# Performance work log

Measured on AMD Instinct MI355X. Metric: run time of the kernel, lower is better.

## Reference

```python
import jax, jax.numpy as jnp
import numpy as np
from jax import ops

N, E, F_IN, H, M, KC, B, C_OUT = 100000, 1600000, 128, 128, 150000, 60000, 64, 10
BN_EPS = 1e-5

def setup_inputs() -> dict:
    key = jax.random.key(0)
    ks = jax.random.split(key, 16)
    s = 0.05
    x = jax.random.normal(ks[0], (N, F_IN), jnp.float32)
    edge_index = jax.random.randint(ks[1], (2, E), 0, N)
    weights = jax.random.uniform(ks[2], (E,), jnp.float32)
    # sorted batch vector covering all B graphs
    batch = (jnp.arange(N) * B) // N
    # cover assignments: every cluster gets at least one node (arange prefix)
    cover_nodes = jax.random.randint(ks[3], (M,), 0, N)
    cover_clusters = jnp.concatenate([jnp.arange(KC), jax.random.randint(ks[4], (M - KC,), 0, KC)])
    cluster_batch = (jnp.arange(KC) * B) // KC
    out_dim = 4 * H  # 2 * num_layers * hidden, readout=True
    return {
        'x': x, 'edge_index': edge_index, 'weights': weights, 'batch': batch,
        'cover_nodes': cover_nodes, 'cover_clusters': cover_clusters, 'cluster_batch': cluster_batch,
        'W_in': jax.random.normal(ks[5], (F_IN, H), jnp.float32) * s,
        'b_in': jnp.zeros((H,), jnp.float32),
        'W_blk': jax.random.normal(ks[6], (2 * H, H), jnp.float32) * s,
        'b_blk': jnp.zeros((H,), jnp.float32),
        'bn_gamma': jnp.ones((out_dim,), jnp.float32),
        'bn_beta': jnp.zeros((out_dim,), jnp.float32),
        'bn_mean': jnp.zeros((out_dim,), jnp.float32),
        'bn_var': jnp.ones((out_dim,), jnp.float32),
        'W1': jax.random.normal(ks[7], (out_dim, H), jnp.float32) * s,
        'b1': jnp.zeros((H,), jnp.float32),
        'W2': jax.random.normal(ks[8], (H, C_OUT), jnp.float32) * s,
        'b2': jnp.zeros((C_OUT,), jnp.float32),
    }

def _gcn(x, src, dst, w, n, W, b):
    # PyG GCNConv: out = D^-1/2 (A + I) D^-1/2 (x W) + b, weighted degrees incl. self loop of 1
    deg = ops.segment_sum(w, dst, num_segments=n) + 1.0
    dinv = jax.lax.rsqrt(deg)
    xw = x @ W
    msg = (w * dinv[src] * dinv[dst])[:, None] * xw[src]          # [E,H]
    agg = ops.segment_sum(msg, dst, num_segments=n) + (dinv * dinv)[:, None] * xw
    return agg + b

def reference(x, edge_index, weights, batch, cover_nodes, cover_clusters, cluster_batch,
              W_in, b_in, W_blk, b_blk, bn_gamma, bn_beta, bn_mean, bn_var, W1, b1, W2, b2):
    src, dst = edge_index[0], edge_index[1]

    # conv_in + relu
    h = jax.nn.relu(_gcn(x, src, dst, weights, N, W_in, b_in))     # [N,H]

    counts = ops.segment_sum(jnp.ones((N,), jnp.float32), batch, num_segments=B)
    xs = [ops.segment_sum(h, batch, num_segments=B),               # global_add_pool
          ops.segment_max(h, batch, num_segments=B)]               # global_max_pool

    # --- pool_graphs: cover_pool_node (add & max) ---
    x_add = ops.segment_sum(h[cover_nodes], cover_clusters, num_segments=KC)
    x_max = ops.segment_max(h[cover_nodes], cover_clusters, num_segments=KC)
    xp = jnp.concatenate([x_add, x_max], axis=1)                   # [KC, 2H]

    # --- pooled GCN, matrix-free A' = C^T A C (cover_pool_edge, pool='add') ---
    def aprime(z):  # z: [KC, d]
        zn = ops.segment_sum(z[cover_clusters], cover_nodes, num_segments=N)   # C z
        ye = ops.segment_sum(weights[:, None] * zn[src], dst, num_segments=N)  # A (C z)
        return ops.segment_sum(ye[cover_nodes], cover_clusters, num_segments=KC)  # C^T ...

    degp = aprime(jnp.ones((KC, 1), jnp.float32))[:, 0] + 1.0      # weighted degree of A'+I
    dinv = jax.lax.rsqrt(degp)
    xw = xp @ W_blk                                                # [KC,H]
    xws = dinv[:, None] * xw
    hp = jax.nn.relu(dinv[:, None] * (aprime(xws) + xws) + b_blk)  # [KC,H]

    ccounts = ops.segment_sum(jnp.ones((KC,), jnp.float32), cluster_batch, num_segments=B)
    xs.append(ops.segment_sum(hp, cluster_batch, num_segments=B) / ccounts[:, None])  # mean pool
    xs.append(ops.segment_max(hp, cluster_batch, num_segments=B))

    z = jnp.concatenate(xs, axis=1)                                # [B, 4H]
    z = (z - bn_mean) * jax.lax.rsqrt(bn_var + BN_EPS) * bn_gamma + bn_beta  # BN (eval)
    z = jax.nn.relu(z @ W1 + b1)                                   # dropout=identity (eval)
    z = z @ W2 + b2
    return jax.nn.softmax(z, axis=-1)
```

## Files before the change

### kernel.cpp

```cpp
#include <hip/hip_runtime.h>


#define H 128
#define TILE_AGG 2048
#define GRID_AGG 784

typedef __attribute__((ext_vector_type(4))) float f32x4;
typedef __attribute__((ext_vector_type(8))) short bf16x8;

__device__ __forceinline__ void atomAddF(float* p, float v) {
    unsafeAtomicAdd(p, v);
}
__device__ __forceinline__ void atomMaxPos(float* p, float v) {
    atomicMax(reinterpret_cast<int*>(p), __float_as_int(v));
}

__device__ __forceinline__ unsigned int bfr(float f) {
    unsigned int u = __float_as_uint(f);
    return (u + 0x7fffu + ((u >> 16) & 1u)) >> 16;
}
__device__ __forceinline__ unsigned int pk2(float lo, float hi) {
    return bfr(lo) | (bfr(hi) << 16);
}
__device__ __forceinline__ float unlo(unsigned int v) { return __uint_as_float(v << 16); }
__device__ __forceinline__ float unhi(unsigned int v) { return __uint_as_float(v & 0xffff0000u); }

__global__ void count_pairs(const int* __restrict__ a, const int* __restrict__ b,
                            int* __restrict__ ca, int* __restrict__ cb, int M) {
    int i = blockIdx.x * blockDim.x + threadIdx.x;
    if (i < M) {
        atomicAdd(&ca[__builtin_nontemporal_load(a + i)], 1);
        atomicAdd(&cb[__builtin_nontemporal_load(b + i)], 1);
    }
}

__global__ __launch_bounds__(256) void scan_partial(const int* __restrict__ c,
                                                    int* __restrict__ part, int m) {
    __shared__ int red[4];
    int base = blockIdx.x * 1024, t = threadIdx.x;
    int s = 0;
    for (int j = t; j < 1024; j += 256) { int i = base + j; if (i < m) s += c[i]; }
    for (int o = 32; o; o >>= 1) s += __shfl_down(s, o, 64);
    if ((t & 63) == 0) red[t >> 6] = s;
    __syncthreads();
    if (t == 0) part[blockIdx.x] = red[0] + red[1] + red[2] + red[3];
}
__global__ void scan_spine(int* part, int G) {
    if (threadIdx.x == 0) {
        int acc = 0;
        for (int i = 0; i < G; ++i) { int v = part[i]; part[i] = acc; acc += v; }
    }
}
__global__ __launch_bounds__(256) void scan_apply(int* __restrict__ c,
                                                  const int* __restrict__ part, int m) {
    __shared__ int wsum[4];
    int base = blockIdx.x * 1024, t = threadIdx.x;
    int i0 = base + t * 4;
    int v0 = 0, v1 = 0, v2 = 0, v3 = 0;
    if (i0     < m) v0 = c[i0];
    if (i0 + 1 < m) v1 = c[i0 + 1];
    if (i0 + 2 < m) v2 = c[i0 + 2];
    if (i0 + 3 < m) v3 = c[i0 + 3];
    int ts = v0 + v1 + v2 + v3;
    int lane = t & 63, w = t >> 6;
    int sc = ts;
    for (int o = 1; o < 64; o <<= 1) { int u = __shfl_up(sc, o, 64); if (lane >= o) sc += u; }
    if (lane == 63) wsum[w] = sc;
    __syncthreads();
    int off = part[blockIdx.x];
    for (int k = 0; k < w; ++k) off += wsum[k];
    int ex = off + sc - ts;
    if (i0     < m) c[i0]     = ex;
    if (i0 + 1 < m) c[i0 + 1] = ex + v0;
    if (i0 + 2 < m) c[i0 + 2] = ex + v0 + v1;
    if (i0 + 3 < m) c[i0 + 3] = ex + v0 + v1 + v2;
}

__global__ void fill_pairs(const int* __restrict__ key, const int* __restrict__ val,
                           int* __restrict__ offs, int* __restrict__ slots, int M) {
    int i = blockIdx.x * blockDim.x + threadIdx.x;
    int p0 = i * 2, p1 = p0 + 1;
    if (p0 >= M) return;
    int k0 = __builtin_nontemporal_load(key + p0);
    int v0 = __builtin_nontemporal_load(val + p0);
    bool has1 = p1 < M;
    int k1 = k0, v1 = 0;
    if (has1) {
        k1 = __builtin_nontemporal_load(key + p1);
        v1 = __builtin_nontemporal_load(val + p1);
    }
    int q0 = atomicAdd(&offs[k0], 1);
    int q1 = has1 ? atomicAdd(&offs[k1], 1) : 0;
    slots[q0] = v0;
    if (has1) slots[q1] = v1;
}

__global__ void qcnt_kernel(const int* __restrict__ qoffs, int* __restrict__ qcnt, int N) {
    int n = blockIdx.x * blockDim.x + threadIdx.x;
    if (n < N) qcnt[n] = qoffs[n] - (n ? qoffs[n - 1] : 0);
}

__global__ __launch_bounds__(256) void hist_coarse(const int* __restrict__ dst,
                                                   int* __restrict__ histc, int E, int Ppad) {
    __shared__ int hb[512];
    for (int i = threadIdx.x; i < 512; i += 256) hb[i] = 0;
    __syncthreads();
    int x = blockIdx.x & 7;
    for (int tile = blockIdx.x; (long)tile * TILE_AGG < E; tile += GRID_AGG) {
        int base = tile * TILE_AGG;
        int lim = min(TILE_AGG, E - base);
        for (int i = threadIdx.x; i < lim; i += 256)
            atomicAdd(&hb[__builtin_nontemporal_load(dst + base + i) >> 8], 1);
    }
    __syncthreads();
    for (int i = threadIdx.x; i < 512; i += 256)
        if (hb[i]) atomicAdd(&histc[x * Ppad + i], hb[i]);
}

__global__ __launch_bounds__(1024) void scan_small(
    const int* __restrict__ histc, int* __restrict__ curscan,
    int* __restrict__ curw, int P, int Ppad)
{
    __shared__ int wtot[16];
    int t = threadIdx.x;
    int m = P * 8;
    int i0 = t * 4;
    int v[4];
#pragma unroll
    for (int k = 0; k < 4; ++k) {
        int id = i0 + k;
        v[k] = (id < m) ? histc[(id & 7) * Ppad + (id >> 3)] : 0;
    }
    int ts = v[0] + v[1] + v[2] + v[3];
    int lane = t & 63, w = t >> 6;
    int sc = ts;
    for (int o = 1; o < 64; o <<= 1) { int u = __shfl_up(sc, o, 64); if (lane >= o) sc += u; }
    if (lane == 63) wtot[w] = sc;
    __syncthreads();
    int off = 0;
    for (int k = 0; k < w; ++k) off += wtot[k];
    int ex = off + sc - ts;
#pragma unroll
    for (int k = 0; k < 4; ++k) {
        int id = i0 + k;
        if (id < m) {
            curscan[id] = ex;
            curw[(id & 7) * Ppad + (id >> 3)] = ex;
        }
        ex += v[k];
    }
}

__global__ __launch_bounds__(256) void fill_stage_agg(
    const int* __restrict__ src, const int* __restrict__ dst,
    const float* __restrict__ w, int* __restrict__ cur,
    int2* __restrict__ stg, int E, int Ppad)
{
    __shared__ int cnt[512];
    __shared__ int gbase[512];
    int t = threadIdx.x;
    int x = blockIdx.x & 7;
    for (int tile = blockIdx.x; (long)tile * TILE_AGG < E; tile += GRID_AGG) {
        int base = tile * TILE_AGG;
        int lim = min(TILE_AGG, E - base);
        for (int i = t; i < 512; i += 256) cnt[i] = 0;
        __syncthreads();
        for (int i = t; i < lim; i += 256)
            atomicAdd(&cnt[__builtin_nontemporal_load(dst + base + i) >> 8], 1);
        __syncthreads();
        for (int b = t; b < 512; b += 256) {
            int c = cnt[b];
            if (c) gbase[b] = atomicAdd(&cur[x * Ppad + b], c);
        }
        __syncthreads();
        for (int i = t; i < 512; i += 256) cnt[i] = 0;
        __syncthreads();
        for (int i = t; i < lim; i += 256) {
            int d  = __builtin_nontemporal_load(dst + base + i);
            int s  = __builtin_nontemporal_load(src + base + i);
            float wv = __builtin_nontemporal_load(w + base + i);
            int b = d >> 8;
            int r = atomicAdd(&cnt[b], 1);
            stg[gbase[b] + r] = make_int2(s | ((d & 255) << 20), __float_as_int(wv));
        }
        __syncthreads();
    }
}

__global__ __launch_bounds__(1024) void fill_compact(
    const int* __restrict__ curscan, const int2* __restrict__ stg,
    int2* __restrict__ epack, int* __restrict__ ieoffs, int E, int N, int P)
{
    __shared__ int cnt[256];
    __shared__ int wsum[4];
    int b = blockIdx.x, t = threadIdx.x;
    int gs = curscan[b * 8];
    int ge = (b == P - 1) ? E : curscan[(b + 1) * 8];
    if (t < 256) cnt[t] = 0;
    __syncthreads();
    for (int i = gs + t; i < ge; i += 1024)
        atomicAdd(&cnt[(stg[i].x >> 20) & 255], 1);
    __syncthreads();
    int v = 0, sc = 0;
    if (t < 256) {
        v = cnt[t];
        int lane = t & 63;
        sc = v;
        for (int o = 1; o < 64; o <<= 1) { int u = __shfl_up(sc, o, 64); if (lane >= o) sc += u; }
        if (lane == 63) wsum[t >> 6] = sc;
    }
    __syncthreads();
    if (t < 256) {
        int off = 0;
        for (int k = 0; k < (t >> 6); ++k) off += wsum[k];
        int excl = off + sc - v;
        int node = b * 256 + t;
        if (node < N) ieoffs[node] = gs + excl + v;
        cnt[t] = excl;
    }
    __syncthreads();
    for (int i = gs + t; i < ge; i += 1024) {
        int2 pv = stg[i];
        int pos = atomicAdd(&cnt[(pv.x >> 20) & 255], 1);
        epack[gs + pos] = make_int2(pv.x & 0xFFFFF, pv.y);
    }
}

__global__ void node_scalars(const int* __restrict__ eoffs, const int* __restrict__ epack,
                             const int* __restrict__ qcnt,
                             float* __restrict__ dinv, float* __restrict__ ye1, int N) {
    int n = blockIdx.x * blockDim.x + threadIdx.x;
    if (n >= N) return;
    int b = n ? eoffs[n - 1] : 0, e = eoffs[n];
    float dg = 0.f, y = 0.f;
    for (int i = b; i < e; ++i) {
        int2 pk = ((const int2*)epack)[i];
        float w = __int_as_float(pk.y);
        dg += w;
        y += w * (float)qcnt[pk.x];
    }
    dinv[n] = rsqrtf(dg + 1.0f);
    ye1[n] = y;
}
__global__ void cluster_dinvp(const int* __restrict__ poffs, const int* __restrict__ pslots,
                              const float* __restrict__ ye1, float* __restrict__ dinvp, int KC) {
    int c = blockIdx.x * blockDim.x + threadIdx.x;
    if (c >= KC) return;
    int b = c ? poffs[c - 1] : 0, e = poffs[c];
    float s = 0.f;
    for (int i = b; i < e; ++i) s += ye1[pslots[i]];
    dinvp[c] = rsqrtf(s + 1.0f);
}

template <int KSTEPS>
__global__ void prepack_w(const float* __restrict__ W, uint4* __restrict__ wp) {
    int idx = blockIdx.x * blockDim.x + threadIdx.x;
    if (idx >= 8 * KSTEPS * 64) return;
    int l = idx & 63;
    int f = idx >> 6;
    int kb = f % KSTEPS, ct = f / KSTEPS;
    int col = ct * 16 + (l & 15);
    int k0 = kb * 32 + (l >> 4) * 8;
    uint4 u;
    u.x = pk2(W[(k0 + 0) * 128 + col], W[(k0 + 1) * 128 + col]);
    u.y = pk2(W[(k0 + 2) * 128 + col], W[(k0 + 3) * 128 + col]);
    u.z = pk2(W[(k0 + 4) * 128 + col], W[(k0 + 5) * 128 + col]);
    u.w = pk2(W[(k0 + 6) * 128 + col], W[(k0 + 7) * 128 + col]);
    wp[idx] = u;
}

template <int KSTEPS>
__global__ __launch_bounds__(256) void gemm_mfma(
    const float* __restrict__ XA,
    const uint4* __restrict__ wpack, const float* __restrict__ rowscale,
    unsigned short* __restrict__ outb, int nrows)
{
    __shared__ uint4 Wl[8 * KSTEPS * 64];
    int t = threadIdx.x;
    for (int i = t; i < 8 * KSTEPS * 64; i += 256) Wl[i] = wpack[i];
    __syncthreads();

    int l = t & 63, wv = t >> 6;
    int row0 = blockIdx.x * 64 + wv * 16;
    int rr = row0 + (l & 15);
    long rc = (rr < nrows ? rr : nrows - 1);
    int kq = (l >> 4) * 8;

    f32x4 acc[8];
#pragma unroll
    for (int ct = 0; ct < 8; ++ct) acc[ct] = (f32x4)0.f;

#pragma unroll
    for (int kb = 0; kb < KSTEPS; ++kb) {
        const float* p = XA + rc * 128 + kb * 32 + kq;
        float4 a0 = ((const float4*)p)[0];
        float4 a1 = ((const float4*)p)[1];
        union { uint4 u; bf16x8 v; } af;
        af.u.x = pk2(a0.x, a0.y); af.u.y = pk2(a0.z, a0.w);
        af.u.z = pk2(a1.x, a1.y); af.u.w = pk2(a1.z, a1.w);
#pragma unroll
        for (int ct = 0; ct < 8; ++ct) {
            union { uint4 u; bf16x8 v; } bf;
            bf.u = Wl[(ct * KSTEPS + kb) * 64 + l];
            acc[ct] = __builtin_amdgcn_mfma_f32_16x16x32_bf16(af.v, bf.v, acc[ct], 0, 0, 0);
        }
    }

    int rbase = row0 + (l >> 4) * 4;
    float sc[4];
#pragma unroll
    for (int g = 0; g < 4; ++g)
        sc[g] = rowscale ? (rbase + g < nrows ? rowscale[rbase + g] : 1.f) : 1.f;
#pragma unroll
    for (int ct = 0; ct < 8; ++ct) {
        int col = ct * 16 + (l & 15);
#pragma unroll
        for (int g = 0; g < 4; ++g) {
            int r = rbase + g;
            if (r < nrows)
                outb[(long)r * 128 + col] = (unsigned short)bfr(acc[ct][g] * sc[g]);
        }
    }
}

__global__ __launch_bounds__(256) void gemm_mfma_bfA(
    const uint4* __restrict__ XA, const uint4* __restrict__ XB,
    const uint4* __restrict__ wpack, const float* __restrict__ rowscale,
    unsigned short* __restrict__ outb, int nrows)
{
    __shared__ uint4 Wl[8 * 8 * 64];
    int t = threadIdx.x;
    for (int i = t; i < 4096; i += 256) Wl[i] = wpack[i];
    __syncthreads();

    int l = t & 63, wv = t >> 6;
    int row0 = blockIdx.x * 64 + wv * 16;
    int rr = row0 + (l & 15);
    long rc = (rr < nrows ? rr : nrows - 1);
    int kq8 = (l >> 4);

    f32x4 acc[8];
#pragma unroll
    for (int ct = 0; ct < 8; ++ct) acc[ct] = (f32x4)0.f;

#pragma unroll
    for (int kb = 0; kb < 8; ++kb) {
        const uint4* s = (kb >= 4) ? XB : XA;
        union { uint4 u; bf16x8 v; } af;
        af.u = s[rc * 16 + (kb & 3) * 4 + kq8];
#pragma unroll
        for (int ct = 0; ct < 8; ++ct) {
            union { uint4 u; bf16x8 v; } bf;
            bf.u = Wl[(ct * 8 + kb) * 64 + l];
            acc[ct] = __builtin_amdgcn_mfma_f32_16x16x32_bf16(af.v, bf.v, acc[ct], 0, 0, 0);
        }
    }

    int rbase = row0 + (l >> 4) * 4;
    float sc[4];
#pragma unroll
    for (int g = 0; g < 4; ++g)
        sc[g] = rowscale ? (rbase + g < nrows ? rowscale[rbase + g] : 1.f) : 1.f;
#pragma unroll
    for (int ct = 0; ct < 8; ++ct) {
        int col = ct * 16 + (l & 15);
#pragma unroll
        for (int g = 0; g < 4; ++g) {
            int r = rbase + g;
            if (r < nrows)
                outb[(long)r * 128 + col] = (unsigned short)bfr(acc[ct][g] * sc[g]);
        }
    }
}


__global__ __launch_bounds__(256) void gcn1_gather(
    const int* __restrict__ eoffs, const int* __restrict__ epack,
    const float* __restrict__ dinv, const uint4* __restrict__ X4,
    const float* __restrict__ bin, uint4* __restrict__ H4, int N)
{
    int n = blockIdx.x * 4 + (threadIdx.x >> 6);
    if (n >= N) return;
    int lane = threadIdx.x & 63;
    int ql = lane & 15, grp = lane >> 4;
    int b = n ? eoffs[n - 1] : 0, e = eoffs[n];
    float4 a0 = make_float4(0.f, 0.f, 0.f, 0.f), a1 = a0;
    for (int i = b; i < e; i += 64) {
        int cnt = min(64, e - i);
        int s_l = 0; float sc_l = 0.f;
        if (lane < cnt) {
            int2 pk = ((const int2*)epack)[i + lane];
            s_l = pk.x;
            sc_l = __int_as_float(pk.y) * dinv[pk.x];
        }
        int steps = (cnt + 3) >> 2;
#pragma unroll 2
        for (int j = 0; j < steps; ++j) {
            int idx = 4 * j + grp;
            int s = __shfl(s_l, idx, 64);
            float sc = __shfl(sc_l, idx, 64);
            uint4 v = X4[(long)s * 16 + ql];
            a0.x += sc * unlo(v.x); a0.y += sc * unhi(v.x);
            a0.z += sc * unlo(v.y); a0.w += sc * unhi(v.y);
            a1.x += sc * unlo(v.z); a1.y += sc * unhi(v.z);
            a1.z += sc * unlo(v.w); a1.w += sc * unhi(v.w);
        }
    }
#pragma unroll
    for (int o = 16; o <= 32; o <<= 1) {
        a0.x += __shfl_xor(a0.x, o, 64); a0.y += __shfl_xor(a0.y, o, 64);
        a0.z += __shfl_xor(a0.z, o, 64); a0.w += __shfl_xor(a0.w, o, 64);
        a1.x += __shfl_xor(a1.x, o, 64); a1.y += __shfl_xor(a1.y, o, 64);
        a1.z += __shfl_xor(a1.z, o, 64); a1.w += __shfl_xor(a1.w, o, 64);
    }
    if (grp == 0) {
        float dd = dinv[n];
        uint4 sv = X4[(long)n * 16 + ql];
        float4 b0 = ((const float4*)bin)[ql * 2];
        float4 b1 = ((const float4*)bin)[ql * 2 + 1];
        float o0 = fmaxf(dd * (a0.x + dd * unlo(sv.x)) + b0.x, 0.f);
        float o1 = fmaxf(dd * (a0.y + dd * unhi(sv.x)) + b0.y, 0.f);
        float o2 = fmaxf(dd * (a0.z + dd * unlo(sv.y)) + b0.z, 0.f);
        float o3 = fmaxf(dd * (a0.w + dd * unhi(sv.y)) + b0.w, 0.f);
        float o4 = fmaxf(dd * (a1.x + dd * unlo(sv.z)) + b1.x, 0.f);
        float o5 = fmaxf(dd * (a1.y + dd * unhi(sv.z)) + b1.y, 0.f);
        float o6 = fmaxf(dd * (a1.z + dd * unlo(sv.w)) + b1.z, 0.f);
        float o7 = fmaxf(dd * (a1.w + dd * unhi(sv.w)) + b1.w, 0.f);
        H4[(long)n * 16 + ql] = make_uint4(pk2(o0, o1), pk2(o2, o3),
                                           pk2(o4, o5), pk2(o6, o7));
    }
}

__global__ __launch_bounds__(256) void edge_gather_plain(
    const int* __restrict__ eoffs, const int* __restrict__ epack,
    const uint4* __restrict__ X4, uint4* __restrict__ Out4, int N)
{
    int n = blockIdx.x * 4 + (threadIdx.x >> 6);
    if (n >= N) return;
    int lane = threadIdx.x & 63;
    int ql = lane & 15, grp = lane >> 4;
    int b = n ? eoffs[n - 1] : 0, e = eoffs[n];
    float4 a0 = make_float4(0.f, 0.f, 0.f, 0.f), a1 = a0;
    for (int i = b; i < e; i += 64) {
        int cnt = min(64, e - i);
        int s_l = 0; float sc_l = 0.f;
        if (lane < cnt) {
            int2 pk = ((const int2*)epack)[i + lane];
            s_l = pk.x; sc_l = __int_as_float(pk.y);
        }
        int steps = (cnt + 3) >> 2;
#pragma unroll 2
        for (int j = 0; j < steps; ++j) {
            int idx = 4 * j + grp;
            int s = __shfl(s_l, idx, 64);
            float sc = __shfl(sc_l, idx, 64);
            uint4 v = X4[(long)s * 16 + ql];
            a0.x += sc * unlo(v.x); a0.y += sc * unhi(v.x);
            a0.z += sc * unlo(v.y); a0.w += sc * unhi(v.y);
            a1.x += sc * unlo(v.z); a1.y += sc * unhi(v.z);
            a1.z += sc * unlo(v.w); a1.w += sc * unhi(v.w);
        }
    }
#pragma unroll
    for (int o = 16; o <= 32; o <<= 1) {
        a0.x += __shfl_xor(a0.x, o, 64); a0.y += __shfl_xor(a0.y, o, 64);
        a0.z += __shfl_xor(a0.z, o, 64); a0.w += __shfl_xor(a0.w, o, 64);
        a1.x += __shfl_xor(a1.x, o, 64); a1.y += __shfl_xor(a1.y, o, 64);
        a1.z += __shfl_xor(a1.z, o, 64); a1.w += __shfl_xor(a1.w, o, 64);
    }
    if (grp == 0)
        Out4[(long)n * 16 + ql] = make_uint4(pk2(a0.x, a0.y), pk2(a0.z, a0.w),
                                             pk2(a1.x, a1.y), pk2(a1.z, a1.w));
}

__global__ __launch_bounds__(256) void cover_pool(
    const int* __restrict__ poffs, const int* __restrict__ pslots,
    const uint4* __restrict__ H4, uint4* __restrict__ xadd,
    uint4* __restrict__ xmax, int KC)
{
    int c = blockIdx.x * 16 + (threadIdx.x >> 4);
    if (c >= KC) return;
    int ql = threadIdx.x & 15;
    int b = c ? poffs[c - 1] : 0, e = poffs[c];
    float4 s0 = make_float4(0.f, 0.f, 0.f, 0.f), s1 = s0, m0 = s0, m1 = s0;
#pragma unroll 2
    for (int i = b; i < e; ++i) {
        uint4 v = H4[(long)pslots[i] * 16 + ql];
        float e0 = unlo(v.x), e1 = unhi(v.x), e2 = unlo(v.y), e3 = unhi(v.y);
        float e4 = unlo(v.z), e5 = unhi(v.z), e6 = unlo(v.w), e7 = unhi(v.w);
        s0.x += e0; s0.y += e1; s0.z += e2; s0.w += e3;
        s1.x += e4; s1.y += e5; s1.z += e6; s1.w += e7;
        m0.x = fmaxf(m0.x, e0); m0.y = fmaxf(m0.y, e1);
        m0.z = fmaxf(m0.z, e2); m0.w = fmaxf(m0.w, e3);
        m1.x = fmaxf(m1.x, e4); m1.y = fmaxf(m1.y, e5);
        m1.z = fmaxf(m1.z, e6); m1.w = fmaxf(m1.w, e7);
    }
    xadd[(long)c * 16 + ql] = make_uint4(pk2(s0.x, s0.y), pk2(s0.z, s0.w),
                                         pk2(s1.x, s1.y), pk2(s1.z, s1.w));
    xmax[(long)c * 16 + ql] = make_uint4(pk2(m0.x, m0.y), pk2(m0.z, m0.w),
                                         pk2(m1.x, m1.y), pk2(m1.z, m1.w));
}

__global__ __launch_bounds__(256) void zn_gather(
    const int* __restrict__ qoffs, const int* __restrict__ qslots,
    const uint4* __restrict__ X4, uint4* __restrict__ Z4, int N)
{
    int n = blockIdx.x * 16 + (threadIdx.x >> 4);
    if (n >= N) return;
    int ql = threadIdx.x & 15;
    int b = n ? qoffs[n - 1] : 0, e = qoffs[n];
    float4 a0 = make_float4(0.f, 0.f, 0.f, 0.f), a1 = a0;
#pragma unroll 2
    for (int i = b; i < e; ++i) {
        uint4 v = X4[(long)qslots[i] * 16 + ql];
        a0.x += unlo(v.x); a0.y += unhi(v.x); a0.z += unlo(v.y); a0.w += unhi(v.y);
        a1.x += unlo(v.z); a1.y += unhi(v.z); a1.z += unlo(v.w); a1.w += unhi(v.w);
    }
    Z4[(long)n * 16 + ql] = make_uint4(pk2(a0.x, a0.y), pk2(a0.z, a0.w),
                                       pk2(a1.x, a1.y), pk2(a1.z, a1.w));
}

__global__ __launch_bounds__(256) void aphp_gather(
    const int* __restrict__ poffs, const int* __restrict__ pslots,
    const uint4* __restrict__ Y4, const uint4* __restrict__ xws4,
    const float* __restrict__ dinvp, const float* __restrict__ bblk,
    uint4* __restrict__ hp4, int KC)
{
    int c = blockIdx.x * 16 + (threadIdx.x >> 4);
    if (c >= KC) return;
    int ql = threadIdx.x & 15;
    int b = c ? poffs[c - 1] : 0, e = poffs[c];
    float4 a0 = make_float4(0.f, 0.f, 0.f, 0.f), a1 = a0;
#pragma unroll 2
    for (int i = b; i < e; ++i) {
        uint4 v = Y4[(long)pslots[i] * 16 + ql];
        a0.x += unlo(v.x); a0.y += unhi(v.x); a0.z += unlo(v.y); a0.w += unhi(v.y);
        a1.x += unlo(v.z); a1.y += unhi(v.z); a1.z += unlo(v.w); a1.w += unhi(v.w);
    }
    float d = dinvp[c];
    uint4 xv = xws4[(long)c * 16 + ql];
    float4 b0 = ((const float4*)bblk)[ql * 2];
    float4 b1 = ((const float4*)bblk)[ql * 2 + 1];
    float o0 = fmaxf(d * (a0.x + unlo(xv.x)) + b0.x, 0.f);
    float o1 = fmaxf(d * (a0.y + unhi(xv.x)) + b0.y, 0.f);
    float o2 = fmaxf(d * (a0.z + unlo(xv.y)) + b0.z, 0.f);
    float o3 = fmaxf(d * (a0.w + unhi(xv.y)) + b0.w, 0.f);
    float o4 = fmaxf(d * (a1.x + unlo(xv.z)) + b1.x, 0.f);
    float o5 = fmaxf(d * (a1.y + unhi(xv.z)) + b1.y, 0.f);
    float o6 = fmaxf(d * (a1.z + unlo(xv.w)) + b1.z, 0.f);
    float o7 = fmaxf(d * (a1.w + unhi(xv.w)) + b1.w, 0.f);
    hp4[(long)c * 16 + ql] = make_uint4(pk2(o0, o1), pk2(o2, o3),
                                        pk2(o4, o5), pk2(o6, o7));
}

__global__ __launch_bounds__(128) void seg_pool_bf(
    const unsigned short* __restrict__ X, const int* __restrict__ seg,
    float* __restrict__ Z, int n, int sumoff, int maxoff)
{
    int j = threadIdx.x;
    long beg = (long)blockIdx.x * n / gridDim.x;
    long end = (long)(blockIdx.x + 1) * n / gridDim.x;
    if (beg >= end) return;
    int curb = seg[beg];
    float s = 0.f, mx = 0.f;
    for (long i = beg; i < end; ++i) {
        int b = seg[i];
        if (b != curb) {
            atomAddF(&Z[(long)curb * 512 + sumoff + j], s);
            atomMaxPos(&Z[(long)curb * 512 + maxoff + j], mx);
            s = 0.f; mx = 0.f; curb = b;
        }
        float v = __uint_as_float((unsigned int)X[i * (long)H + j] << 16);
        s += v; mx = fmaxf(mx, v);
    }
    atomAddF(&Z[(long)curb * 512 + sumoff + j], s);
    atomMaxPos(&Z[(long)curb * 512 + maxoff + j], mx);
}

__global__ void hist64(const int* __restrict__ seg, float* __restrict__ cc, int n) {
    __shared__ int hc[128];
    if (threadIdx.x < 128) hc[threadIdx.x] = 0;
    __syncthreads();
    for (int i = blockIdx.x * blockDim.x + threadIdx.x; i < n; i += gridDim.x * blockDim.x)
        atomicAdd(&hc[seg[i]], 1);
    __syncthreads();
    if (threadIdx.x < 128 && hc[threadIdx.x] != 0)
        atomAddF(&cc[threadIdx.x], (float)hc[threadIdx.x]);
}

__global__ __launch_bounds__(128) void head_kernel(
    const float* __restrict__ z, const float* __restrict__ cc,
    const float* __restrict__ gamma, const float* __restrict__ beta,
    const float* __restrict__ bmean, const float* __restrict__ bvar,
    const float* __restrict__ W1, const float* __restrict__ b1,
    const float* __restrict__ W2, const float* __restrict__ b2,
    float* __restrict__ out)
{
    __shared__ float zb[512];
    __shared__ float z1[128];
    __shared__ float lg[10];
    __shared__ float red[2];
    int b = blockIdx.x, t = threadIdx.x;
    float ccb = cc[b];
    for (int k = t; k < 512; k += 128) {
        float v = z[(long)b * 512 + k];
        if (k >= 256 && k < 384) v /= ccb;
        v = (v - bmean[k]) * rsqrtf(bvar[k] + 1e-5f) * gamma[k] + beta[k];
        zb[k] = v;
    }
    __syncthreads();
    float acc = b1[t];
    for (int k = 0; k < 512; ++k) acc += zb[k] * W1[k * 128 + t];
    z1[t] = fmaxf(acc, 0.f);
    __syncthreads();
    if (t < 10) {
        float a = b2[t];
        for (int k = 0; k < 128; ++k) a += z1[k] * W2[k * 10 + t];
        lg[t] = a;
    }
    __syncthreads();
    if (t == 0) {
        float m = lg[0];
        for (int i = 1; i < 10; ++i) m = fmaxf(m, lg[i]);
        float s = 0.f;
        for (int i = 0; i < 10; ++i) s += expf(lg[i] - m);
        red[0] = m; red[1] = s;
    }
    __syncthreads();
    if (t < 10) out[(long)b * 10 + t] = expf(lg[t] - red[0]) / red[1];
}

static void scan_ex(int* buf, int m, int* part, hipStream_t s) {
    int G = (m + 1023) / 1024;
    scan_partial<<<G, 256, 0, s>>>(buf, part, m);
    scan_spine<<<1, 64, 0, s>>>(part, G);
    scan_apply<<<G, 256, 0, s>>>(buf, part, m);
}

extern "C" void kernel_launch(void* const* d_in, const int* in_sizes, int n_in,
                              void* d_out, int out_size, void* d_ws, size_t ws_size,
                              hipStream_t stream)
{
    const float* x      = (const float*)d_in[0];
    const int*   ei     = (const int*)  d_in[1];
    const float* wts    = (const float*)d_in[2];
    const int*   batch  = (const int*)  d_in[3];
    const int*   cnodes = (const int*)  d_in[4];
    const int*   cclus  = (const int*)  d_in[5];
    const int*   cbatch = (const int*)  d_in[6];
    const float* Win    = (const float*)d_in[7];
    const float* bin    = (const float*)d_in[8];
    const float* Wblk   = (const float*)d_in[9];
    const float* bblk   = (const float*)d_in[10];
    const float* gma    = (const float*)d_in[11];
    const float* bta    = (const float*)d_in[12];
    const float* bmean  = (const float*)d_in[13];
    const float* bvar   = (const float*)d_in[14];
    const float* W1     = (const float*)d_in[15];
    const float* b1     = (const float*)d_in[16];
    const float* W2     = (const float*)d_in[17];
    const float* b2     = (const float*)d_in[18];
    float* out = (float*)d_out;

    const int N  = in_sizes[0] / H;
    const int E  = in_sizes[1] / 2;
    const int M  = in_sizes[4];
    const int KC = in_sizes[6];
    const int Bq = out_size / 10;
    const int P  = (N + 255) >> 8;
    const int Ppad = (P + 15) & ~15;

    const int* src = ei;
    const int* dst = ei + E;

    const long NH = (long)N * H;
    const long KH = (long)KC * H;

    float* ws     = (float*)d_ws;
    uint4* wpackN = (uint4*)ws;
    uint4* wpackK = wpackN + 2048;
    unsigned int* Abf = (unsigned int*)(wpackK + 4096);
    unsigned int* Hbf = Abf + NH / 2;
    unsigned int* Cbf = Hbf + NH / 2;
    unsigned int* Fadd= Cbf + KH / 2;
    unsigned int* Fmax= Fadd + KH / 2;
    float* dinv = (float*)(Fmax + KH / 2);
    float* ye1  = dinv + N;
    float* dinvp= ye1 + N;
    float* z    = dinvp + KC;
    float* cc   = z + (long)Bq * 512;
    int* ieoffs = (int*)(cc + Bq);
    int* ipoffs = ieoffs + N;
    int* iqoffs = ipoffs + KC;
    int* epack  = iqoffs + N;
    int* pslots = epack + 2L * E;
    int* qslots = pslots + M;
    int* spart  = qslots + M;
    int* curscan= spart + 2048;
    int* histc  = curscan + P * 8;
    int* curw   = histc + 8 * Ppad;
    int* qcnt   = curw + 8 * Ppad;
    int2* estg  = (int2*)(qcnt + N);

    hipMemsetAsync(histc, 0, 8 * Ppad * sizeof(int), stream);
    hist_coarse<<<GRID_AGG, 256, 0, stream>>>(dst, histc, E, Ppad);
    scan_small<<<1, 1024, 0, stream>>>(histc, curscan, curw, P, Ppad);
    fill_stage_agg<<<GRID_AGG, 256, 0, stream>>>(src, dst, wts, curw, estg, E, Ppad);
    fill_compact<<<P, 1024, 0, stream>>>(curscan, estg, (int2*)epack, ieoffs, E, N, P);

    hipMemsetAsync(ipoffs, 0, ((long)KC + N) * sizeof(int), stream);
    count_pairs<<<(M + 255) / 256, 256, 0, stream>>>(cclus, cnodes, ipoffs, iqoffs, M);
    scan_ex(ipoffs, KC, spart, stream);
    scan_ex(iqoffs, N, spart, stream);
    fill_pairs<<<(M / 2 + 256) / 256, 256, 0, stream>>>(cclus, cnodes, ipoffs, pslots, M);
    fill_pairs<<<(M / 2 + 256) / 256, 256, 0, stream>>>(cnodes, cclus, iqoffs, qslots, M);
    qcnt_kernel<<<(N + 255) / 256, 256, 0, stream>>>(iqoffs, qcnt, N);

    prepack_w<4><<<8, 256, 0, stream>>>(Win, wpackN);
    prepack_w<8><<<16, 256, 0, stream>>>(Wblk, wpackK);

    node_scalars<<<(N + 255) / 256, 256, 0, stream>>>(ieoffs, epack, qcnt, dinv, ye1, N);
    cluster_dinvp<<<(KC + 255) / 256, 256, 0, stream>>>(ipoffs, pslots, ye1, dinvp, KC);

    gemm_mfma<4><<<(N + 63) / 64, 256, 0, stream>>>(x, wpackN, nullptr,
                                                    (unsigned short*)Abf, N);
    gcn1_gather<<<(N + 3) / 4, 256, 0, stream>>>(ieoffs, epack, dinv,
                                                 (const uint4*)Abf, bin,
                                                 (uint4*)Hbf, N);

    hipMemsetAsync(z, 0, ((long)Bq * 512 + Bq) * sizeof(float), stream);
    cover_pool<<<(KC + 15) / 16, 256, 0, stream>>>(ipoffs, pslots, (const uint4*)Hbf,
                                                   (uint4*)Fadd, (uint4*)Fmax, KC);
    seg_pool_bf<<<1024, 128, 0, stream>>>((const unsigned short*)Hbf, batch, z, N, 0, 128);
    hist64<<<256, 256, 0, stream>>>(cbatch, cc, KC);

    gemm_mfma_bfA<<<(KC + 63) / 64, 256, 0, stream>>>((const uint4*)Fadd, (const uint4*)Fmax,
                                                      wpackK, dinvp,
                                                      (unsigned short*)Cbf, KC);

    zn_gather<<<(N + 15) / 16, 256, 0, stream>>>(iqoffs, qslots, (const uint4*)Cbf,
                                                 (uint4*)Abf, N);
    edge_gather_plain<<<(N + 3) / 4, 256, 0, stream>>>(ieoffs, epack,
                                                       (const uint4*)Abf,
                                                       (uint4*)Hbf, N);
    aphp_gather<<<(KC + 15) / 16, 256, 0, stream>>>(ipoffs, pslots, (const uint4*)Hbf,
                                                    (const uint4*)Cbf, dinvp, bblk,
                                                    (uint4*)Fadd, KC);

    seg_pool_bf<<<512, 128, 0, stream>>>((const unsigned short*)Fadd, cbatch, z, KC, 256, 384);
    head_kernel<<<Bq, 128, 0, stream>>>(z, cc, gma, bta, bmean, bvar, W1, b1, W2, b2, out);
}
```

Measured before the change: 455.3 us.

## Fuse node scalars into CSR compaction, merge pair fills, stage GEMM stores, nontemporal I/O

Computes weighted degree and the ye1 sum inside fill_compact using shared-memory float atomics, removing the separate node_scalars pass over the edge list. The cover CSR build is moved ahead of the edge CSR build so that qcnt is ready, and the two fill_pairs launches are merged into one. GEMM epilogues now stage bf16 results in LDS and write coalesced 16-byte nontemporal stores. Gather kernels use nontemporal loads and stores and 32-bit index arithmetic. Shared float atomics make the degree sums order-nondeterministic, and the staged epilogue adds a barrier and reuses the weight LDS buffer.

```diff
diff --git a/kernel.cpp b/kernel.cpp
--- a/kernel.cpp
+++ b/kernel.cpp
@@ -7,6 +7,7 @@
 
 typedef __attribute__((ext_vector_type(4))) float f32x4;
 typedef __attribute__((ext_vector_type(8))) short bf16x8;
+typedef __attribute__((ext_vector_type(4))) unsigned int u32x4;
 
 __device__ __forceinline__ void atomAddF(float* p, float v) {
     unsafeAtomicAdd(p, v);
@@ -24,6 +25,12 @@
 }
 __device__ __forceinline__ float unlo(unsigned int v) { return __uint_as_float(v << 16); }
 __device__ __forceinline__ float unhi(unsigned int v) { return __uint_as_float(v & 0xffff0000u); }
+
+__device__ __forceinline__ void ntstore4(unsigned int a, unsigned int b,
+                                         unsigned int c, unsigned int d, void* p) {
+    u32x4 v; v.x = a; v.y = b; v.z = c; v.w = d;
+    __builtin_nontemporal_store(v, (u32x4*)p);
+}
 
 __global__ void count_pairs(const int* __restrict__ a, const int* __restrict__ b,
                             int* __restrict__ ca, int* __restrict__ cb, int M) {
@@ -76,23 +83,17 @@
     if (i0 + 3 < m) c[i0 + 3] = ex + v0 + v1 + v2;
 }
 
-__global__ void fill_pairs(const int* __restrict__ key, const int* __restrict__ val,
-                           int* __restrict__ offs, int* __restrict__ slots, int M) {
+__global__ void fill_pairs_both(const int* __restrict__ cclus, const int* __restrict__ cnodes,
+                                int* __restrict__ ipoffs, int* __restrict__ iqoffs,
+                                int* __restrict__ pslots, int* __restrict__ qslots, int M) {
     int i = blockIdx.x * blockDim.x + threadIdx.x;
-    int p0 = i * 2, p1 = p0 + 1;
-    if (p0 >= M) return;
-    int k0 = __builtin_nontemporal_load(key + p0);
-    int v0 = __builtin_nontemporal_load(val + p0);
-    bool has1 = p1 < M;
-    int k1 = k0, v1 = 0;
-    if (has1) {
-        k1 = __builtin_nontemporal_load(key + p1);
-        v1 = __builtin_nontemporal_load(val + p1);
-    }
-    int q0 = atomicAdd(&offs[k0], 1);
-    int q1 = has1 ? atomicAdd(&offs[k1], 1) : 0;
-    slots[q0] = v0;
-    if (has1) slots[q1] = v1;
+    if (i >= M) return;
+    int c = __builtin_nontemporal_load(cclus + i);
+    int n = __builtin_nontemporal_load(cnodes + i);
+    int qp = atomicAdd(&ipoffs[c], 1);
+    int qq = atomicAdd(&iqoffs[n], 1);
+    pslots[qp] = n;
+    qslots[qq] = c;
 }
 
 __global__ void qcnt_kernel(const int* __restrict__ qoffs, int* __restrict__ qcnt, int N) {
@@ -189,17 +190,28 @@
 
 __global__ __launch_bounds__(1024) void fill_compact(
     const int* __restrict__ curscan, const int2* __restrict__ stg,
-    int2* __restrict__ epack, int* __restrict__ ieoffs, int E, int N, int P)
+    int2* __restrict__ epack, int* __restrict__ ieoffs,
+    const int* __restrict__ qcnt, float* __restrict__ dinv,
+    float* __restrict__ ye1, int E, int N, int P)
 {
     __shared__ int cnt[256];
+    __shared__ float degw[256];
+    __shared__ float ysum[256];
     __shared__ int wsum[4];
     int b = blockIdx.x, t = threadIdx.x;
     int gs = curscan[b * 8];
     int ge = (b == P - 1) ? E : curscan[(b + 1) * 8];
-    if (t < 256) cnt[t] = 0;
-    __syncthreads();
-    for (int i = gs + t; i < ge; i += 1024)
-        atomicAdd(&cnt[(stg[i].x >> 20) & 255], 1);
+    if (t < 256) { cnt[t] = 0; degw[t] = 0.f; ysum[t] = 0.f; }
+    __syncthreads();
+    for (int i = gs + t; i < ge; i += 1024) {
+        int2 pv = stg[i];
+        int dloc = (pv.x >> 20) & 255;
+        int s = pv.x & 0xFFFFF;
+        float w = __int_as_float(pv.y);
+        atomicAdd(&cnt[dloc], 1);
+        atomicAdd(&degw[dloc], w);
+        atomicAdd(&ysum[dloc], w * (float)qcnt[s]);
+    }
     __syncthreads();
     int v = 0, sc = 0;
     if (t < 256) {
@@ -215,7 +227,11 @@
         for (int k = 0; k < (t >> 6); ++k) off += wsum[k];
         int excl = off + sc - v;
         int node = b * 256 + t;
-        if (node < N) ieoffs[node] = gs + excl + v;
+        if (node < N) {
+            ieoffs[node] = gs + excl + v;
+            dinv[node] = rsqrtf(degw[t] + 1.0f);
+            ye1[node] = ysum[t];
+        }
         cnt[t] = excl;
     }
     __syncthreads();
@@ -226,22 +242,6 @@
     }
 }
 
-__global__ void node_scalars(const int* __restrict__ eoffs, const int* __restrict__ epack,
-                             const int* __restrict__ qcnt,
-                             float* __restrict__ dinv, float* __restrict__ ye1, int N) {
-    int n = blockIdx.x * blockDim.x + threadIdx.x;
-    if (n >= N) return;
-    int b = n ? eoffs[n - 1] : 0, e = eoffs[n];
-    float dg = 0.f, y = 0.f;
-    for (int i = b; i < e; ++i) {
-        int2 pk = ((const int2*)epack)[i];
-        float w = __int_as_float(pk.y);
-        dg += w;
-        y += w * (float)qcnt[pk.x];
-    }
-    dinv[n] = rsqrtf(dg + 1.0f);
-    ye1[n] = y;
-}
 __global__ void cluster_dinvp(const int* __restrict__ poffs, const int* __restrict__ pslots,
                               const float* __restrict__ ye1, float* __restrict__ dinvp, int KC) {
     int c = blockIdx.x * blockDim.x + threadIdx.x;
@@ -269,6 +269,34 @@
     wp[idx] = u;
 }
 
+__device__ __forceinline__ void gemm_epilogue(
+    unsigned short* Sl, f32x4 (&acc)[8], const float* rowscale,
+    unsigned short* outb, int nrows, int t, int l, int wv, int row0)
+{
+    int rbase = row0 + (l >> 4) * 4;
+    float sc[4];
+#pragma unroll
+    for (int g = 0; g < 4; ++g)
+        sc[g] = rowscale ? (rbase + g < nrows ? rowscale[rbase + g] : 1.f) : 1.f;
+    int lr = wv * 16 + (l >> 4) * 4;
+#pragma unroll
+    for (int ct = 0; ct < 8; ++ct) {
+        int col = ct * 16 + (l & 15);
+#pragma unroll
+        for (int g = 0; g < 4; ++g)
+            Sl[(lr + g) * 128 + col] = (unsigned short)bfr(acc[ct][g] * sc[g]);
+    }
+    __syncthreads();
+    long rowbase = (long)(row0 - wv * 16);
+    u32x4* out4 = (u32x4*)outb;
+    const u32x4* S4 = (const u32x4*)Sl;
+    for (int idx = t; idx < 64 * 16; idx += 256) {
+        long gr = rowbase + (idx >> 4);
+        if (gr < nrows)
+            __builtin_nontemporal_store(S4[idx], &out4[gr * 16 + (idx & 15)]);
+    }
+}
+
 template <int KSTEPS>
 __global__ __launch_bounds__(256) void gemm_mfma(
     const float* __restrict__ XA,
@@ -305,22 +333,8 @@
             acc[ct] = __builtin_amdgcn_mfma_f32_16x16x32_bf16(af.v, bf.v, acc[ct], 0, 0, 0);
         }
     }
-
-    int rbase = row0 + (l >> 4) * 4;
-    float sc[4];
-#pragma unroll
-    for (int g = 0; g < 4; ++g)
-        sc[g] = rowscale ? (rbase + g < nrows ? rowscale[rbase + g] : 1.f) : 1.f;
-#pragma unroll
-    for (int ct = 0; ct < 8; ++ct) {
-        int col = ct * 16 + (l & 15);
-#pragma unroll
-        for (int g = 0; g < 4; ++g) {
-            int r = rbase + g;
-            if (r < nrows)
-                outb[(long)r * 128 + col] = (unsigned short)bfr(acc[ct][g] * sc[g]);
-        }
-    }
+    __syncthreads();
+    gemm_epilogue((unsigned short*)Wl, acc, rowscale, outb, nrows, t, l, wv, row0);
 }
 
 __global__ __launch_bounds__(256) void gemm_mfma_bfA(
@@ -355,27 +369,13 @@
             acc[ct] = __builtin_amdgcn_mfma_f32_16x16x32_bf16(af.v, bf.v, acc[ct], 0, 0, 0);
         }
     }
-
-    int rbase = row0 + (l >> 4) * 4;
-    float sc[4];
-#pragma unroll
-    for (int g = 0; g < 4; ++g)
-        sc[g] = rowscale ? (rbase + g < nrows ? rowscale[rbase + g] : 1.f) : 1.f;
-#pragma unroll
-    for (int ct = 0; ct < 8; ++ct) {
-        int col = ct * 16 + (l & 15);
-#pragma unroll
-        for (int g = 0; g < 4; ++g) {
-            int r = rbase + g;
-            if (r < nrows)
-                outb[(long)r * 128 + col] = (unsigned short)bfr(acc[ct][g] * sc[g]);
-        }
-    }
+    __syncthreads();
+    gemm_epilogue((unsigned short*)Wl, acc, rowscale, outb, nrows, t, l, wv, row0);
 }
 
 
 __global__ __launch_bounds__(256) void gcn1_gather(
-    const int* __restrict__ eoffs, const int* __restrict__ epack,
+    const int* __restrict__ eoffs, const long long* __restrict__ epack,
     const float* __restrict__ dinv, const uint4* __restrict__ X4,
     const float* __restrict__ bin, uint4* __restrict__ H4, int N)
 {
@@ -389,9 +389,9 @@
         int cnt = min(64, e - i);
         int s_l = 0; float sc_l = 0.f;
         if (lane < cnt) {
-            int2 pk = ((const int2*)epack)[i + lane];
-            s_l = pk.x;
-            sc_l = __int_as_float(pk.y) * dinv[pk.x];
+            long long pk8 = __builtin_nontemporal_load(epack + i + lane);
+            s_l = (int)(pk8 & 0xffffffff);
+            sc_l = __int_as_float((int)(pk8 >> 32)) * dinv[s_l];
         }
         int steps = (cnt + 3) >> 2;
 #pragma unroll 2
@@ -399,7 +399,7 @@
             int idx = 4 * j + grp;
             int s = __shfl(s_l, idx, 64);
             float sc = __shfl(sc_l, idx, 64);
-            uint4 v = X4[(long)s * 16 + ql];
+            uint4 v = X4[(unsigned)s * 16u + ql];
             a0.x += sc * unlo(v.x); a0.y += sc * unhi(v.x);
             a0.z += sc * unlo(v.y); a0.w += sc * unhi(v.y);
             a1.x += sc * unlo(v.z); a1.y += sc * unhi(v.z);
@@ -415,7 +415,7 @@
     }
     if (grp == 0) {
         float dd = dinv[n];
-        uint4 sv = X4[(long)n * 16 + ql];
+        uint4 sv = X4[(unsigned)n * 16u + ql];
         float4 b0 = ((const float4*)bin)[ql * 2];
         float4 b1 = ((const float4*)bin)[ql * 2 + 1];
         float o0 = fmaxf(dd * (a0.x + dd * unlo(sv.x)) + b0.x, 0.f);
@@ -426,13 +426,13 @@
         float o5 = fmaxf(dd * (a1.y + dd * unhi(sv.z)) + b1.y, 0.f);
         float o6 = fmaxf(dd * (a1.z + dd * unlo(sv.w)) + b1.z, 0.f);
         float o7 = fmaxf(dd * (a1.w + dd * unhi(sv.w)) + b1.w, 0.f);
-        H4[(long)n * 16 + ql] = make_uint4(pk2(o0, o1), pk2(o2, o3),
-                                           pk2(o4, o5), pk2(o6, o7));
+        ntstore4(pk2(o0, o1), pk2(o2, o3), pk2(o4, o5), pk2(o6, o7),
+                 &H4[(long)n * 16 + ql]);
     }
 }
 
 __global__ __launch_bounds__(256) void edge_gather_plain(
-    const int* __restrict__ eoffs, const int* __restrict__ epack,
+    const int* __restrict__ eoffs, const long long* __restrict__ epack,
     const uint4* __restrict__ X4, uint4* __restrict__ Out4, int N)
 {
     int n = blockIdx.x * 4 + (threadIdx.x >> 6);
@@ -445,8 +445,9 @@
         int cnt = min(64, e - i);
         int s_l = 0; float sc_l = 0.f;
         if (lane < cnt) {
-            int2 pk = ((const int2*)epack)[i + lane];
-            s_l = pk.x; sc_l = __int_as_float(pk.y);
+            long long pk8 = __builtin_nontemporal_load(epack + i + lane);
+            s_l = (int)(pk8 & 0xffffffff);
+            sc_l = __int_as_float((int)(pk8 >> 32));
         }
         int steps = (cnt + 3) >> 2;
 #pragma unroll 2
@@ -454,7 +455,7 @@
             int idx = 4 * j + grp;
             int s = __shfl(s_l, idx, 64);
             float sc = __shfl(sc_l, idx, 64);
-            uint4 v = X4[(long)s * 16 + ql];
+            uint4 v = X4[(unsigned)s * 16u + ql];
             a0.x += sc * unlo(v.x); a0.y += sc * unhi(v.x);
             a0.z += sc * unlo(v.y); a0.w += sc * unhi(v.y);
             a1.x += sc * unlo(v.z); a1.y += sc * unhi(v.z);
@@ -469,8 +470,8 @@
         a1.z += __shfl_xor(a1.z, o, 64); a1.w += __shfl_xor(a1.w, o, 64);
     }
     if (grp == 0)
-        Out4[(long)n * 16 + ql] = make_uint4(pk2(a0.x, a0.y), pk2(a0.z, a0.w),
-                                             pk2(a1.x, a1.y), pk2(a1.z, a1.w));
+        ntstore4(pk2(a0.x, a0.y), pk2(a0.z, a0.w), pk2(a1.x, a1.y), pk2(a1.z, a1.w),
+                 &Out4[(long)n * 16 + ql]);
 }
 
 __global__ __launch_bounds__(256) void cover_pool(
@@ -485,7 +486,7 @@
     float4 s0 = make_float4(0.f, 0.f, 0.f, 0.f), s1 = s0, m0 = s0, m1 = s0;
 #pragma unroll 2
     for (int i = b; i < e; ++i) {
-        uint4 v = H4[(long)pslots[i] * 16 + ql];
+        uint4 v = H4[(unsigned)__builtin_nontemporal_load(pslots + i) * 16u + ql];
         float e0 = unlo(v.x), e1 = unhi(v.x), e2 = unlo(v.y), e3 = unhi(v.y);
         float e4 = unlo(v.z), e5 = unhi(v.z), e6 = unlo(v.w), e7 = unhi(v.w);
         s0.x += e0; s0.y += e1; s0.z += e2; s0.w += e3;
@@ -495,10 +496,10 @@
         m1.x = fmaxf(m1.x, e4); m1.y = fmaxf(m1.y, e5);
         m1.z = fmaxf(m1.z, e6); m1.w = fmaxf(m1.w, e7);
     }
-    xadd[(long)c * 16 + ql] = make_uint4(pk2(s0.x, s0.y), pk2(s0.z, s0.w),
-                                         pk2(s1.x, s1.y), pk2(s1.z, s1.w));
-    xmax[(long)c * 16 + ql] = make_uint4(pk2(m0.x, m0.y), pk2(m0.z, m0.w),
-                                         pk2(m1.x, m1.y), pk2(m1.z, m1.w));
+    ntstore4(pk2(s0.x, s0.y), pk2(s0.z, s0.w), pk2(s1.x, s1.y), pk2(s1.z, s1.w),
+             &xadd[(long)c * 16 + ql]);
+    ntstore4(pk2(m0.x, m0.y), pk2(m0.z, m0.w), pk2(m1.x, m1.y), pk2(m1.z, m1.w),
+             &xmax[(long)c * 16 + ql]);
 }
 
 __global__ __launch_bounds__(256) void zn_gather(
@@ -512,12 +513,12 @@
     float4 a0 = make_float4(0.f, 0.f, 0.f, 0.f), a1 = a0;
 #pragma unroll 2
     for (int i = b; i < e; ++i) {
-        uint4 v = X4[(long)qslots[i] * 16 + ql];
+        uint4 v = X4[(unsigned)__builtin_nontemporal_load(qslots + i) * 16u + ql];
         a0.x += unlo(v.x); a0.y += unhi(v.x); a0.z += unlo(v.y); a0.w += unhi(v.y);
         a1.x += unlo(v.z); a1.y += unhi(v.z); a1.z += unlo(v.w); a1.w += unhi(v.w);
     }
-    Z4[(long)n * 16 + ql] = make_uint4(pk2(a0.x, a0.y), pk2(a0.z, a0.w),
-                                       pk2(a1.x, a1.y), pk2(a1.z, a1.w));
+    ntstore4(pk2(a0.x, a0.y), pk2(a0.z, a0.w), pk2(a1.x, a1.y), pk2(a1.z, a1.w),
+             &Z4[(long)n * 16 + ql]);
 }
 
 __global__ __launch_bounds__(256) void aphp_gather(
@@ -533,7 +534,7 @@
     float4 a0 = make_float4(0.f, 0.f, 0.f, 0.f), a1 = a0;
 #pragma unroll 2
     for (int i = b; i < e; ++i) {
-        uint4 v = Y4[(long)pslots[i] * 16 + ql];
+        uint4 v = Y4[(unsigned)__builtin_nontemporal_load(pslots + i) * 16u + ql];
         a0.x += unlo(v.x); a0.y += unhi(v.x); a0.z += unlo(v.y); a0.w += unhi(v.y);
         a1.x += unlo(v.z); a1.y += unhi(v.z); a1.z += unlo(v.w); a1.w += unhi(v.w);
     }
@@ -549,8 +550,8 @@
     float o5 = fmaxf(d * (a1.y + unhi(xv.z)) + b1.y, 0.f);
     float o6 = fmaxf(d * (a1.z + unlo(xv.w)) + b1.z, 0.f);
     float o7 = fmaxf(d * (a1.w + unhi(xv.w)) + b1.w, 0.f);
-    hp4[(long)c * 16 + ql] = make_uint4(pk2(o0, o1), pk2(o2, o3),
-                                        pk2(o4, o5), pk2(o6, o7));
+    ntstore4(pk2(o0, o1), pk2(o2, o3), pk2(o4, o5), pk2(o6, o7),
+             &hp4[(long)c * 16 + ql]);
 }
 
 __global__ __launch_bounds__(128) void seg_pool_bf(
@@ -702,29 +703,28 @@
     int* qcnt   = curw + 8 * Ppad;
     int2* estg  = (int2*)(qcnt + N);
 
+    hipMemsetAsync(ipoffs, 0, ((long)KC + N) * sizeof(int), stream);
+    count_pairs<<<(M + 255) / 256, 256, 0, stream>>>(cclus, cnodes, ipoffs, iqoffs, M);
+    scan_ex(ipoffs, KC, spart, stream);
+    scan_ex(iqoffs, N, spart, stream);
+    fill_pairs_both<<<(M + 255) / 256, 256, 0, stream>>>(cclus, cnodes, ipoffs, iqoffs,
+                                                         pslots, qslots, M);
+    qcnt_kernel<<<(N + 255) / 256, 256, 0, stream>>>(iqoffs, qcnt, N);
+
     hipMemsetAsync(histc, 0, 8 * Ppad * sizeof(int), stream);
     hist_coarse<<<GRID_AGG, 256, 0, stream>>>(dst, histc, E, Ppad);
     scan_small<<<1, 1024, 0, stream>>>(histc, curscan, curw, P, Ppad);
     fill_stage_agg<<<GRID_AGG, 256, 0, stream>>>(src, dst, wts, curw, estg, E, Ppad);
-    fill_compact<<<P, 1024, 0, stream>>>(curscan, estg, (int2*)epack, ieoffs, E, N, P);
-
-    hipMemsetAsync(ipoffs, 0, ((long)KC + N) * sizeof(int), stream);
-    count_pairs<<<(M + 255) / 256, 256, 0, stream>>>(cclus, cnodes, ipoffs, iqoffs, M);
-    scan_ex(ipoffs, KC, spart, stream);
-    scan_ex(iqoffs, N, spart, stream);
-    fill_pairs<<<(M / 2 + 256) / 256, 256, 0, stream>>>(cclus, cnodes, ipoffs, pslots, M);
-    fill_pairs<<<(M / 2 + 256) / 256, 256, 0, stream>>>(cnodes, cclus, iqoffs, qslots, M);
-    qcnt_kernel<<<(N + 255) / 256, 256, 0, stream>>>(iqoffs, qcnt, N);
+    fill_compact<<<P, 1024, 0, stream>>>(curscan, estg, (int2*)epack, ieoffs,
+                                         qcnt, dinv, ye1, E, N, P);
+    cluster_dinvp<<<(KC + 255) / 256, 256, 0, stream>>>(ipoffs, pslots, ye1, dinvp, KC);
 
     prepack_w<4><<<8, 256, 0, stream>>>(Win, wpackN);
     prepack_w<8><<<16, 256, 0, stream>>>(Wblk, wpackK);
 
-    node_scalars<<<(N + 255) / 256, 256, 0, stream>>>(ieoffs, epack, qcnt, dinv, ye1, N);
-    cluster_dinvp<<<(KC + 255) / 256, 256, 0, stream>>>(ipoffs, pslots, ye1, dinvp, KC);
-
     gemm_mfma<4><<<(N + 63) / 64, 256, 0, stream>>>(x, wpackN, nullptr,
                                                     (unsigned short*)Abf, N);
-    gcn1_gather<<<(N + 3) / 4, 256, 0, stream>>>(ieoffs, epack, dinv,
+    gcn1_gather<<<(N + 3) / 4, 256, 0, stream>>>(ieoffs, (const long long*)epack, dinv,
                                                  (const uint4*)Abf, bin,
                                                  (uint4*)Hbf, N);
 
@@ -740,7 +740,7 @@
 
     zn_gather<<<(N + 15) / 16, 256, 0, stream>>>(iqoffs, qslots, (const uint4*)Cbf,
                                                  (uint4*)Abf, N);
-    edge_gather_plain<<<(N + 3) / 4, 256, 0, stream>>>(ieoffs, epack,
+    edge_gather_plain<<<(N + 3) / 4, 256, 0, stream>>>(ieoffs, (const long long*)epack,
                                                        (const uint4*)Abf,
                                                        (uint4*)Hbf, N);
     aphp_gather<<<(KC + 15) / 16, 256, 0, stream>>>(ipoffs, pslots, (const uint4*)Hbf,
```

Result: slower. 472.0 us, median of 2 (+3.7%).
